# Optimization experiments

Measured on AMD Instinct MI355X. Metric: run time of the kernel, lower is better.

Reference implementation:

```python
import jax, jax.numpy as jnp
import numpy as np

B, S, D_IN, D_INT, D_OUT, E, K_SYN = 2, 2048, 2048, 2048, 2048, 4, 512
GROUPS = D_INT // 8  # Conv1d groups

def setup_inputs() -> dict:
    key = jax.random.key(0)
    ks = jax.random.split(key, 20)
    n = lambda k, sh, std: jax.random.normal(k, sh, dtype=jnp.float32) * std
    d = {}
    d['x'] = jax.random.normal(ks[0], (B, S, D_IN), dtype=jnp.float32)
    d['syntax_ids'] = jax.random.randint(ks[1], (B, S), 0, K_SYN, dtype=jnp.int32)
    d['W_in'] = n(ks[2], (D_IN, D_INT), D_IN ** -0.5)
    d['b_in'] = jnp.zeros((D_INT,), jnp.float32)
    d['W_syn_emb'] = n(ks[3], (K_SYN, D_INT // 4), 0.02)
    d['W_syn'] = n(ks[4], (D_INT + D_INT // 4, D_INT), 0.02)
    d['b_syn'] = jnp.zeros((D_INT,), jnp.float32)
    d['W_gate'] = n(ks[5], (D_INT, 1), 0.02)
    d['b_gate'] = jnp.zeros((1,), jnp.float32)
    d['W_router'] = n(ks[6], (D_INT, E), 0.02)
    d['b_router'] = jnp.zeros((E,), jnp.float32)
    d['W_e1'] = n(ks[7], (E, D_INT, 2 * D_INT), 0.02)
    d['b_e1'] = jnp.zeros((E, 2 * D_INT), jnp.float32)
    d['W_e2'] = n(ks[8], (E, 2 * D_INT, D_INT), 0.02)
    d['b_e2'] = jnp.zeros((E, D_INT), jnp.float32)
    d['W_ctx'] = n(ks[9], (D_INT, D_INT), D_INT ** -0.5)
    d['b_ctx'] = jnp.zeros((D_INT,), jnp.float32)
    fan = 8 * 3 + 8 * 3
    lim = float(np.sqrt(6.0 / fan))
    d['conv_w'] = jax.random.uniform(ks[10], (D_INT, 8, 3), jnp.float32, -lim, lim)
    d['conv_b'] = jnp.zeros((D_INT,), jnp.float32)
    d['W_out'] = n(ks[11], (D_INT, D_OUT), D_INT ** -0.5)
    d['b_out'] = jnp.zeros((D_OUT,), jnp.float32)
    return d

def _forward(x, syntax_ids, W_in, b_in, W_syn_emb, W_syn, b_syn, W_gate, b_gate,
             W_router, b_router, W_e1, b_e1, W_e2, b_e2, W_ctx, b_ctx,
             conv_w, conv_b, W_out, b_out):
    # input projection + SiLU (dropout is identity in eval / p=0)
    h = jax.nn.silu(jnp.einsum('bsi,id->bsd', x, W_in) + b_in)
    # syntax-aware projection
    se = W_syn_emb[syntax_ids]                       # [B,S,D/4] gather
    h = jnp.einsum('bsc,cd->bsd', jnp.concatenate([h, se], axis=-1), W_syn) + b_syn
    # adaptive computation gate
    gate = jax.nn.sigmoid(jnp.einsum('bsd,do->bso', h, W_gate) + b_gate)
    h = h * gate
    # dense mixture-of-experts combine (softmax router weights)
    probs = jax.nn.softmax(jnp.einsum('bsd,de->bse', h, W_router) + b_router, axis=-1)
    eh = jax.nn.silu(jnp.einsum('bsd,edf->bsef', h, W_e1) + b_e1)   # [B,S,E,2D]
    eo = jnp.einsum('bsef,efd->bsed', eh, W_e2) + b_e2              # [B,S,E,D]
    h = h + jnp.einsum('bsed,bse->bsd', eo, probs)
    # code-specific: context linear + grouped Conv1d pattern extractor
    ctx = jnp.einsum('bsd,df->bsf', h, W_ctx) + b_ctx
    hc = jnp.transpose(h, (0, 2, 1))  # [B,D,S]
    pat = jax.lax.conv_general_dilated(
        hc, conv_w, window_strides=(1,), padding=((1, 1),),
        dimension_numbers=('NCH', 'OIH', 'NCH'), feature_group_count=GROUPS)
    pat = jnp.transpose(pat + conv_b[None, :, None], (0, 2, 1))
    h = h + ctx + pat
    out = jnp.einsum('bsd,do->bso', h, W_out) + b_out
    return out + x  # residual (input_dim == output_dim)

def reference(x, syntax_ids, W_in, b_in, W_syn_emb, W_syn, b_syn, W_gate, b_gate,
              W_router, b_router, W_e1, b_e1, W_e2, b_e2, W_ctx, b_ctx,
              conv_w, conv_b, W_out, b_out):
    return _forward(x, syntax_ids, W_in, b_in, W_syn_emb, W_syn, b_syn, W_gate,
                    b_gate, W_router, b_router, W_e1, b_e1, W_e2, b_e2,
                    W_ctx, b_ctx, conv_w, conv_b, W_out, b_out)
```

## Files before the change

### kernel.cpp

```cpp
#include <hip/hip_runtime.h>

typedef __attribute__((ext_vector_type(8))) short short8;
typedef __attribute__((ext_vector_type(4))) float floatx4;

#define BM 128
#define BN 128
#define BK 32

__device__ __forceinline__ float b2f(ushort us) {
    union { unsigned u; float f; } v; v.u = ((unsigned)us) << 16; return v.f;
}
__device__ __forceinline__ ushort f2b(float f) {
    union { float f; unsigned u; } v; v.f = f;
    unsigned r = (v.u + 0x7fffu + ((v.u >> 16) & 1u)) >> 16;
    return (ushort)r;
}
__device__ __forceinline__ float ldany(const void* p, long i, int bf) {
    return bf ? b2f(((const ushort*)p)[i]) : ((const float*)p)[i];
}
__device__ __forceinline__ void async16(const ushort* g, ushort* l) {
    __builtin_amdgcn_global_load_lds((const __attribute__((address_space(1))) void*)g,
                                     (__attribute__((address_space(3))) void*)l,
                                     16, 0, 0);
}

__global__ void detect_dtype(const unsigned* __restrict__ w, int* __restrict__ flag)
{
    if (threadIdx.x == 0 && blockIdx.x == 0) {
        int votes = 0;
        for (int i = 0; i < 256; i++) {
            unsigned e = (w[i] >> 7) & 0xFFu;
            if (e >= 112u && e <= 128u) votes++;
        }
        *flag = (votes >= 128) ? 1 : 0;
    }
}

__global__ __launch_bounds__(256) void transpose_any(
    const void* __restrict__ in, long in_off, ushort* __restrict__ out,
    int R, int C, const int* __restrict__ flag)
{
    __shared__ float tile[64][65];
    const int bf = *flag;
    const int t  = threadIdx.x;
    const long r0 = (long)blockIdx.y * 64;
    const long c0 = (long)blockIdx.x * 64;
    const int rl = t >> 4;
    const int cl = (t & 15) * 4;
    #pragma unroll
    for (int p = 0; p < 4; p++) {
        const int r = rl + p * 16;
        const long base = in_off + (r0 + r) * C + c0 + cl;
        if (bf) {
            ushort4 v = *(const ushort4*)((const ushort*)in + base);
            tile[r][cl + 0] = b2f(v.x); tile[r][cl + 1] = b2f(v.y);
            tile[r][cl + 2] = b2f(v.z); tile[r][cl + 3] = b2f(v.w);
        } else {
            float4 v = *(const float4*)((const float*)in + base);
            tile[r][cl + 0] = v.x; tile[r][cl + 1] = v.y;
            tile[r][cl + 2] = v.z; tile[r][cl + 3] = v.w;
        }
    }
    __syncthreads();
    #pragma unroll
    for (int p = 0; p < 4; p++) {
        const int oc = rl + p * 16;
        ushort4 v;
        v.x = f2b(tile[cl + 0][oc]); v.y = f2b(tile[cl + 1][oc]);
        v.z = f2b(tile[cl + 2][oc]); v.w = f2b(tile[cl + 3][oc]);
        *(ushort4*)(out + (c0 + oc) * R + r0 + cl) = v;
    }
}

__global__ void to_bf16_any(const void* __restrict__ in, ushort* __restrict__ out,
                            long n4, const int* __restrict__ flag)
{
    const long i = (long)blockIdx.x * blockDim.x + threadIdx.x;
    if (i >= n4) return;
    const int bf = *flag;
    ushort4 o;
    if (bf) {
        o = ((const ushort4*)in)[i];
    } else {
        float4 v = ((const float4*)in)[i];
        o.x = f2b(v.x); o.y = f2b(v.y); o.z = f2b(v.z); o.w = f2b(v.w);
    }
    ((ushort4*)out)[i] = o;
}

__global__ void f32_to_bf16_4(const float* __restrict__ in, ushort* __restrict__ out, long n4)
{
    const long i = (long)blockIdx.x * blockDim.x + threadIdx.x;
    if (i >= n4) return;
    float4 v = ((const float4*)in)[i];
    ushort4 o; o.x = f2b(v.x); o.y = f2b(v.y); o.z = f2b(v.z); o.w = f2b(v.w);
    ((ushort4*)out)[i] = o;
}

#define EPI_SILU   0
#define EPI_BIAS   1
#define EPI_EXPERT 2
#define EPI_CTX    3
#define EPI_OUT    4

template<int EPI>
__global__ __launch_bounds__(256, 2) void gemm_bt(
    const ushort* __restrict__ A, const ushort* __restrict__ Bt,
    int M, int N, int K,
    const void* __restrict__ bias, long bias_off,
    void* __restrict__ out, long ldo,
    float* __restrict__ hacc,
    const float* __restrict__ rowscale,
    const ushort* __restrict__ resid,
    const int* __restrict__ flag)
{
    __shared__ __align__(16) ushort As[BM * BK];
    __shared__ __align__(16) ushort Bs[BN * BK];

    const int tid  = threadIdx.x;
    const int lane = tid & 63;
    const int wv   = tid >> 6;
    const int wm   = wv & 1;
    const int wn   = wv >> 1;
    const long m0  = (long)blockIdx.y * BM;
    const long n0  = (long)blockIdx.x * BN;

    floatx4 acc[4][4] = {};

    const int sr = (lane >> 2);
    const int sk = (lane & 3) * 8;
    const ushort* Ag = A  + (m0 + wv * 32 + sr) * (long)K + sk;
    const ushort* Bg = Bt + (n0 + wv * 32 + sr) * (long)K + sk;
    ushort* Al = As + (wv * 32) * BK;
    ushort* Bl = Bs + (wv * 32) * BK;

    const int fr = lane & 15;
    const int q  = lane >> 4;
    const ushort* ApL = As + (wm * 64 + fr) * BK + q * 8;
    const ushort* BpL = Bs + (wn * 64 + fr) * BK + q * 8;

    for (int k0 = 0; k0 < K; k0 += BK) {
        __syncthreads();
        async16(Ag + k0,            Al);
        async16(Ag + 16L * K + k0,  Al + 16 * BK);
        async16(Bg + k0,            Bl);
        async16(Bg + 16L * K + k0,  Bl + 16 * BK);
        __syncthreads();
        short8 af[4], bfr[4];
        #pragma unroll
        for (int i = 0; i < 4; i++) af[i]  = *(const short8*)(ApL + i * 16 * BK);
        #pragma unroll
        for (int j = 0; j < 4; j++) bfr[j] = *(const short8*)(BpL + j * 16 * BK);
        #pragma unroll
        for (int i = 0; i < 4; i++)
            #pragma unroll
            for (int j = 0; j < 4; j++)
                acc[i][j] = __builtin_amdgcn_mfma_f32_16x16x32_bf16(
                                af[i], bfr[j], acc[i][j], 0, 0, 0);
    }

    const int bf = *flag;
    #pragma unroll
    for (int i = 0; i < 4; i++) {
        #pragma unroll
        for (int r = 0; r < 4; r++) {
            const long m = m0 + wm * 64 + i * 16 + q * 4 + r;
            #pragma unroll
            for (int j = 0; j < 4; j++) {
                const long n = n0 + wn * 64 + j * 16 + fr;
                float v = acc[i][j][r] + ldany(bias, bias_off + n, bf);
                if (EPI == EPI_SILU) {
                    v = v / (1.f + __expf(-v));
                    ((ushort*)out)[m * ldo + n] = f2b(v);
                } else if (EPI == EPI_BIAS) {
                    ((ushort*)out)[m * ldo + n] = f2b(v);
                } else if (EPI == EPI_EXPERT) {
                    hacc[m * (long)N + n] += rowscale[m * 4] * v;
                } else if (EPI == EPI_CTX) {
                    hacc[m * (long)N + n] += v;
                } else {
                    v += b2f(resid[m * (long)N + n]);
                    if (bf) ((ushort*)out)[m * ldo + n] = f2b(v);
                    else    ((float*)out)[m * ldo + n]  = v;
                }
            }
        }
    }
}

__global__ void gather_syn(const int* __restrict__ ids, const void* __restrict__ emb,
                           ushort* __restrict__ hA, const int* __restrict__ flag)
{
    const int bf = *flag;
    const long m = blockIdx.x;
    const int id = ids[m];
    const int j = threadIdx.x * 2;
    float a, b;
    if (bf) {
        ushort2 v = *(const ushort2*)((const ushort*)emb + (long)id * 512 + j);
        a = b2f(v.x); b = b2f(v.y);
    } else {
        float2 v = *(const float2*)((const float*)emb + (long)id * 512 + j);
        a = v.x; b = v.y;
    }
    ushort2 o; o.x = f2b(a); o.y = f2b(b);
    *(ushort2*)(hA + m * 2560 + 2048 + j) = o;
}

__global__ __launch_bounds__(256) void gate_router(
    ushort* __restrict__ h2, float* __restrict__ hacc, float* __restrict__ probs,
    const void* __restrict__ Wg, const void* __restrict__ bg,
    const void* __restrict__ Wr, const void* __restrict__ br,
    const int* __restrict__ flag)
{
    const int bf = *flag;
    const long m = blockIdx.x;
    const int t = threadIdx.x;
    const int lane = t & 63;
    const int wv = t >> 6;
    ushort* row = h2 + m * 2048;

    float sg = 0.f, s0 = 0.f, s1 = 0.f, s2 = 0.f, s3 = 0.f;
    for (int k = t; k < 2048; k += 256) {
        const float h = b2f(row[k]);
        sg += h * ldany(Wg, k, bf);
        float r0v, r1v, r2v, r3v;
        if (bf) {
            ushort4 v = *(const ushort4*)((const ushort*)Wr + (long)k * 4);
            r0v = b2f(v.x); r1v = b2f(v.y); r2v = b2f(v.z); r3v = b2f(v.w);
        } else {
            float4 v = *(const float4*)((const float*)Wr + (long)k * 4);
            r0v = v.x; r1v = v.y; r2v = v.z; r3v = v.w;
        }
        s0 += h * r0v; s1 += h * r1v; s2 += h * r2v; s3 += h * r3v;
    }
    #pragma unroll
    for (int off = 32; off > 0; off >>= 1) {
        sg += __shfl_down(sg, off);
        s0 += __shfl_down(s0, off);
        s1 += __shfl_down(s1, off);
        s2 += __shfl_down(s2, off);
        s3 += __shfl_down(s3, off);
    }
    __shared__ float red[4][5];
    __shared__ float gate_bc;
    if (lane == 0) {
        red[wv][0] = sg; red[wv][1] = s0; red[wv][2] = s1;
        red[wv][3] = s2; red[wv][4] = s3;
    }
    __syncthreads();
    if (t == 0) {
        float G = red[0][0] + red[1][0] + red[2][0] + red[3][0];
        float R[4];
        #pragma unroll
        for (int e = 0; e < 4; e++)
            R[e] = red[0][1 + e] + red[1][1 + e] + red[2][1 + e] + red[3][1 + e];
        const float gate = 1.f / (1.f + __expf(-(G + ldany(bg, 0, bf))));
        float lg[4], mx = -1e30f;
        #pragma unroll
        for (int e = 0; e < 4; e++) {
            lg[e] = gate * R[e] + ldany(br, e, bf);
            mx = fmaxf(mx, lg[e]);
        }
        float p[4], s = 0.f;
        #pragma unroll
        for (int e = 0; e < 4; e++) { p[e] = __expf(lg[e] - mx); s += p[e]; }
        #pragma unroll
        for (int e = 0; e < 4; e++) probs[m * 4 + e] = p[e] / s;
        gate_bc = gate;
    }
    __syncthreads();
    const float gate = gate_bc;
    for (int k = t; k < 2048; k += 256) {
        const float v = b2f(row[k]) * gate;
        row[k] = f2b(v);
        hacc[m * 2048 + k] = v;
    }
}

__global__ __launch_bounds__(256) void conv_combine(
    const ushort* __restrict__ h4, const float* __restrict__ hacc,
    const void* __restrict__ cw, const void* __restrict__ cb,
    ushort* __restrict__ h5, const int* __restrict__ flag)
{
    const int S = 2048, D = 2048;
    const int bf = *flag;
    const int b = blockIdx.z, g = blockIdx.y;
    const int s0 = blockIdx.x * 64;
    __shared__ float tile[66 * 8];
    const int t = threadIdx.x;
    for (int idx = t; idx < 66 * 8; idx += 256) {
        const int sl = idx >> 3, i = idx & 7;
        const int s = s0 + sl - 1;
        float v = 0.f;
        if (s >= 0 && s < S) v = b2f(h4[((long)b * S + s) * D + g * 8 + i]);
        tile[idx] = v;
    }
    __syncthreads();
    const int io = t & 7;
    const int c = g * 8 + io;
    float w[3][8];
    #pragma unroll
    for (int kk = 0; kk < 3; kk++)
        #pragma unroll
        for (int ii = 0; ii < 8; ii++)
            w[kk][ii] = ldany(cw, (long)c * 24 + ii * 3 + kk, bf);
    const float bc = ldany(cb, c, bf);
    #pragma unroll
    for (int p = 0; p < 2; p++) {
        const int sl = (t >> 3) + p * 32;
        float pat = 0.f;
        #pragma unroll
        for (int kk = 0; kk < 3; kk++)
            #pragma unroll
            for (int ii = 0; ii < 8; ii++)
                pat += tile[(sl + kk) * 8 + ii] * w[kk][ii];
        const long m = (long)b * S + s0 + sl;
        h5[m * D + c] = f2b(hacc[m * D + c] + bc + pat);
    }
}

extern "C" void kernel_launch(void* const* d_in, const int* in_sizes, int n_in,
                              void* d_out, int out_size, void* d_ws, size_t ws_size,
                              hipStream_t stream)
{
    (void)in_sizes; (void)n_in; (void)out_size; (void)ws_size;
    const void* x        = d_in[0];
    const int*  syn      = (const int*)d_in[1];
    const void* W_in     = d_in[2];
    const void* b_in     = d_in[3];
    const void* W_synemb = d_in[4];
    const void* W_syn    = d_in[5];
    const void* b_syn    = d_in[6];
    const void* W_gate   = d_in[7];
    const void* b_gate   = d_in[8];
    const void* W_router = d_in[9];
    const void* b_router = d_in[10];
    const void* W_e1     = d_in[11];
    const void* b_e1     = d_in[12];
    const void* W_e2     = d_in[13];
    const void* b_e2     = d_in[14];
    const void* W_ctx    = d_in[15];
    const void* b_ctx    = d_in[16];
    const void* conv_w   = d_in[17];
    const void* conv_b   = d_in[18];
    const void* W_out    = d_in[19];
    const void* b_out    = d_in[20];

    char* ws = (char*)d_ws;
    int*    flag  = (int*)ws;
    ushort* WT    = (ushort*)(ws + 256);
    ushort* xb    = (ushort*)(ws + 16777472);
    ushort* hA    = (ushort*)(ws + 33554688);
    ushort* eh    = (ushort*)(ws + 16777472);
    ushort* h23   = (ushort*)(ws + 54526208);
    float*  probs = (float*)(ws + 71303424);
    float*  hacc  = (float*)(ws + 71368960);
    const int M = 4096;
    dim3 blk(256);

    detect_dtype<<<dim3(1), dim3(64), 0, stream>>>((const unsigned*)W_in, flag);
    to_bf16_any<<<dim3(8192), blk, 0, stream>>>(x, xb, 2097152L, flag);

    transpose_any<<<dim3(32, 32), blk, 0, stream>>>(W_in, 0, WT, 2048, 2048, flag);
    gemm_bt<EPI_SILU><<<dim3(16, 32), blk, 0, stream>>>(
        xb, WT, M, 2048, 2048, b_in, 0, hA, 2560, nullptr, nullptr, nullptr, flag);
    gather_syn<<<dim3(4096), blk, 0, stream>>>(syn, W_synemb, hA, flag);
    transpose_any<<<dim3(32, 40), blk, 0, stream>>>(W_syn, 0, WT, 2560, 2048, flag);
    gemm_bt<EPI_BIAS><<<dim3(16, 32), blk, 0, stream>>>(
        hA, WT, M, 2048, 2560, b_syn, 0, h23, 2048, nullptr, nullptr, nullptr, flag);
    gate_router<<<dim3(4096), blk, 0, stream>>>(
        h23, hacc, probs, W_gate, b_gate, W_router, b_router, flag);
    for (int e = 0; e < 4; e++) {
        transpose_any<<<dim3(64, 32), blk, 0, stream>>>(
            W_e1, (long)e * 8388608, WT, 2048, 4096, flag);
        gemm_bt<EPI_SILU><<<dim3(32, 32), blk, 0, stream>>>(
            h23, WT, M, 4096, 2048, b_e1, (long)e * 4096, eh, 4096,
            nullptr, nullptr, nullptr, flag);
        transpose_any<<<dim3(32, 64), blk, 0, stream>>>(
            W_e2, (long)e * 8388608, WT, 4096, 2048, flag);
        gemm_bt<EPI_EXPERT><<<dim3(16, 32), blk, 0, stream>>>(
            eh, WT, M, 2048, 4096, b_e2, (long)e * 2048, nullptr, 0,
            hacc, probs + e, nullptr, flag);
    }
    to_bf16_any<<<dim3(8192), blk, 0, stream>>>(x, xb, 2097152L, flag);
    f32_to_bf16_4<<<dim3(8192), blk, 0, stream>>>(hacc, h23, 2097152L);
    transpose_any<<<dim3(32, 32), blk, 0, stream>>>(W_ctx, 0, WT, 2048, 2048, flag);
    gemm_bt<EPI_CTX><<<dim3(16, 32), blk, 0, stream>>>(
        h23, WT, M, 2048, 2048, b_ctx, 0, nullptr, 0, hacc, nullptr, nullptr, flag);
    conv_combine<<<dim3(32, 256, 2), blk, 0, stream>>>(
        h23, hacc, conv_w, conv_b, hA, flag);
    transpose_any<<<dim3(32, 32), blk, 0, stream>>>(W_out, 0, WT, 2048, 2048, flag);
    gemm_bt<EPI_OUT><<<dim3(16, 32), blk, 0, stream>>>(
        hA, WT, M, 2048, 2048, b_out, 0, d_out, 2048, nullptr, nullptr, xb, flag);
}
```

Measured before the change: 1.579 ms.

## Double-buffer GEMM LDS tiles and fuse bf16 snapshot into last expert epilogue

The GEMM main loop now uses two LDS buffers per operand. It prefetches the next K-tile with async global-to-LDS loads while MFMAs run on the current tile, and drops one of the two barriers per iteration. Separately, the final expert GEMM gets a new epilogue that writes the bf16 copy of the accumulated hidden state directly. This removes the standalone f32-to-bf16 conversion pass over hacc. The cost is doubled LDS use per block, which may reduce occupancy, and relying on the single barrier to order the async copies.

Result: no change. 1.584 ms (+0.3%).

```diff
diff --git a/kernel.cpp b/kernel.cpp
--- a/kernel.cpp
+++ b/kernel.cpp
@@ -6,6 +6,8 @@
 #define BM 128
 #define BN 128
 #define BK 32
+#define ABUF (BM * BK)
+#define BBUF (BN * BK)
 
 __device__ __forceinline__ float b2f(ushort us) {
     union { unsigned u; float f; } v; v.u = ((unsigned)us) << 16; return v.f;
@@ -88,20 +90,12 @@
     ((ushort4*)out)[i] = o;
 }
 
-__global__ void f32_to_bf16_4(const float* __restrict__ in, ushort* __restrict__ out, long n4)
-{
-    const long i = (long)blockIdx.x * blockDim.x + threadIdx.x;
-    if (i >= n4) return;
-    float4 v = ((const float4*)in)[i];
-    ushort4 o; o.x = f2b(v.x); o.y = f2b(v.y); o.z = f2b(v.z); o.w = f2b(v.w);
-    ((ushort4*)out)[i] = o;
-}
-
-#define EPI_SILU   0
-#define EPI_BIAS   1
-#define EPI_EXPERT 2
-#define EPI_CTX    3
-#define EPI_OUT    4
+#define EPI_SILU    0
+#define EPI_BIAS    1
+#define EPI_EXPERT  2
+#define EPI_CTX     3
+#define EPI_OUT     4
+#define EPI_EXPSNAP 5
 
 template<int EPI>
 __global__ __launch_bounds__(256, 2) void gemm_bt(
@@ -114,8 +108,8 @@
     const ushort* __restrict__ resid,
     const int* __restrict__ flag)
 {
-    __shared__ __align__(16) ushort As[BM * BK];
-    __shared__ __align__(16) ushort Bs[BN * BK];
+    __shared__ __align__(16) ushort As[2 * ABUF];
+    __shared__ __align__(16) ushort Bs[2 * BBUF];
 
     const int tid  = threadIdx.x;
     const int lane = tid & 63;
@@ -124,6 +118,7 @@
     const int wn   = wv >> 1;
     const long m0  = (long)blockIdx.y * BM;
     const long n0  = (long)blockIdx.x * BN;
+    const int bf   = *flag;
 
     floatx4 acc[4][4] = {};
 
@@ -136,16 +131,26 @@
 
     const int fr = lane & 15;
     const int q  = lane >> 4;
-    const ushort* ApL = As + (wm * 64 + fr) * BK + q * 8;
-    const ushort* BpL = Bs + (wn * 64 + fr) * BK + q * 8;
-
+    const int aoff = (wm * 64 + fr) * BK + q * 8;
+    const int boff = (wn * 64 + fr) * BK + q * 8;
+
+    async16(Ag,            Al);
+    async16(Ag + 16L * K,  Al + 16 * BK);
+    async16(Bg,            Bl);
+    async16(Bg + 16L * K,  Bl + 16 * BK);
+
+    int cur = 0;
     for (int k0 = 0; k0 < K; k0 += BK) {
         __syncthreads();
-        async16(Ag + k0,            Al);
-        async16(Ag + 16L * K + k0,  Al + 16 * BK);
-        async16(Bg + k0,            Bl);
-        async16(Bg + 16L * K + k0,  Bl + 16 * BK);
-        __syncthreads();
+        const int nxt = cur ^ 1;
+        if (k0 + BK < K) {
+            async16(Ag + k0 + BK,            Al + nxt * ABUF);
+            async16(Ag + 16L * K + k0 + BK,  Al + nxt * ABUF + 16 * BK);
+            async16(Bg + k0 + BK,            Bl + nxt * BBUF);
+            async16(Bg + 16L * K + k0 + BK,  Bl + nxt * BBUF + 16 * BK);
+        }
+        const ushort* ApL = As + cur * ABUF + aoff;
+        const ushort* BpL = Bs + cur * BBUF + boff;
         short8 af[4], bfr[4];
         #pragma unroll
         for (int i = 0; i < 4; i++) af[i]  = *(const short8*)(ApL + i * 16 * BK);
@@ -157,9 +162,9 @@
             for (int j = 0; j < 4; j++)
                 acc[i][j] = __builtin_amdgcn_mfma_f32_16x16x32_bf16(
                                 af[i], bfr[j], acc[i][j], 0, 0, 0);
-    }
-
-    const int bf = *flag;
+        cur = nxt;
+    }
+
     #pragma unroll
     for (int i = 0; i < 4; i++) {
         #pragma unroll
@@ -176,6 +181,10 @@
                     ((ushort*)out)[m * ldo + n] = f2b(v);
                 } else if (EPI == EPI_EXPERT) {
                     hacc[m * (long)N + n] += rowscale[m * 4] * v;
+                } else if (EPI == EPI_EXPSNAP) {
+                    const float v2 = hacc[m * (long)N + n] + rowscale[m * 4] * v;
+                    hacc[m * (long)N + n] = v2;
+                    ((ushort*)out)[m * ldo + n] = f2b(v2);
                 } else if (EPI == EPI_CTX) {
                     hacc[m * (long)N + n] += v;
                 } else {
@@ -379,12 +388,16 @@
             nullptr, nullptr, nullptr, flag);
         transpose_any<<<dim3(32, 64), blk, 0, stream>>>(
             W_e2, (long)e * 8388608, WT, 4096, 2048, flag);
-        gemm_bt<EPI_EXPERT><<<dim3(16, 32), blk, 0, stream>>>(
-            eh, WT, M, 2048, 4096, b_e2, (long)e * 2048, nullptr, 0,
-            hacc, probs + e, nullptr, flag);
+        if (e < 3)
+            gemm_bt<EPI_EXPERT><<<dim3(16, 32), blk, 0, stream>>>(
+                eh, WT, M, 2048, 4096, b_e2, (long)e * 2048, nullptr, 0,
+                hacc, probs + e, nullptr, flag);
+        else
+            gemm_bt<EPI_EXPSNAP><<<dim3(16, 32), blk, 0, stream>>>(
+                eh, WT, M, 2048, 4096, b_e2, (long)e * 2048, h23, 2048,
+                hacc, probs + e, nullptr, flag);
     }
     to_bf16_any<<<dim3(8192), blk, 0, stream>>>(x, xb, 2097152L, flag);
-    f32_to_bf16_4<<<dim3(8192), blk, 0, stream>>>(hacc, h23, 2097152L);
     transpose_any<<<dim3(32, 32), blk, 0, stream>>>(W_ctx, 0, WT, 2048, 2048, flag);
     gemm_bt<EPI_CTX><<<dim3(16, 32), blk, 0, stream>>>(
         h23, WT, M, 2048, 2048, b_ctx, 0, nullptr, 0, hacc, nullptr, nullptr, flag);
```
